# Kernel optimization log

Hardware: AMD Instinct MI355X
Metric: run time of the kernel (lower is better)

Reference implementation:

```python
import jax, jax.numpy as jnp
import numpy as np

N_NODES = 50000
N_EDGES = 800000
DIM = 100

def setup_inputs() -> dict:
    key = jax.random.key(0)
    k1, k2, k3, k4, k5, k6 = jax.random.split(key, 6)
    ego_embedding = jax.random.normal(k1, (N_NODES, DIM), dtype=jnp.float32)
    edge_src = jax.random.randint(k2, (N_EDGES,), 0, N_NODES, dtype=jnp.int32)
    edge_dst = jax.random.randint(k3, (N_EDGES,), 0, N_NODES, dtype=jnp.int32)
    edge_weight = jax.random.uniform(k4, (N_EDGES,), dtype=jnp.float32)
    W = jax.random.normal(k5, (DIM, DIM), dtype=jnp.float32) * (1.0 / np.sqrt(DIM))
    b = jax.random.normal(k6, (DIM,), dtype=jnp.float32) * 0.01
    return {"ego_embedding": ego_embedding, "edge_src": edge_src,
            "edge_dst": edge_dst, "edge_weight": edge_weight, "W": W, "b": b}

def reference(ego_embedding, edge_src, edge_dst, edge_weight, W, b):
    # Linear projection: h = x @ W^T + b  (torch Linear convention)
    hidden = ego_embedding @ W.T + b                    # [N, D]
    # u_mul_e: message on each edge = h[src] * edge_weight
    msgs = hidden[edge_src] * edge_weight[:, None]       # [E, D]
    # sum reduce into destination nodes
    out = jax.ops.segment_sum(msgs, edge_dst, num_segments=N_NODES)  # [N, D]
    return out
```

## Files before the change

kernel.cpp:

```cpp
#include <hip/hip_runtime.h>

#define N_NODES 50000
#define N_EDGES 800000
#define DIM 100

#define NB      1563
#define CAPB    768
#define OVF_CAP 4096
#define EPB     8192
#define GEMM_BLOCKS 625
#define BIN_BLOCKS  98
#define ROWS_PB 80

#define HIDB_OFF  0u
#define GCUR_OFF  10000000u
#define OVFC_OFF  10006256u
#define OVF_OFF   10006272u
#define BKT2_OFF  10071808u
#define WT_OFF    19674880u
#define WS_NEED   19714880u

__device__ inline unsigned bf16hi(float v) {
    unsigned u = __float_as_uint(v);
    u += 0x7FFFu + ((u >> 16) & 1u);
    return u & 0xFFFF0000u;
}
__device__ inline unsigned bf16pair(float lo, float hi) {
    unsigned ulo = __float_as_uint(lo); ulo += 0x7FFFu + ((ulo >> 16) & 1u);
    unsigned uhi = __float_as_uint(hi); uhi += 0x7FFFu + ((uhi >> 16) & 1u);
    return (ulo >> 16) | (uhi & 0xFFFF0000u);
}

__global__ __launch_bounds__(256) void srgnn_transpose(
    const float* __restrict__ W, float* __restrict__ Wt,
    int* __restrict__ gcur, int* __restrict__ ovfc)
{
    const unsigned i = blockIdx.x * 256u + threadIdx.x;
    if (i < DIM * DIM) {
        const int c = i / DIM, k = i - c * DIM;
        Wt[k * DIM + c] = W[i];
    }
    if (i < NB) gcur[i] = 0;
    if (i == 0) *ovfc = 0;
}

__global__ __launch_bounds__(512) void srgnn_gemm_bin(
    const float* __restrict__ x, const float* __restrict__ Wt,
    const float* __restrict__ b, unsigned* __restrict__ hidU,
    const int* __restrict__ esrc, const int* __restrict__ edst,
    const float* __restrict__ ew, int* __restrict__ gcur,
    int* __restrict__ ovfc, int4* __restrict__ ovf, uint2* __restrict__ bkt2)
{
    __shared__ __align__(16) char smem[32000];
    const int t = threadIdx.x;

    if (blockIdx.x < GEMM_BLOCKS) {
        float (*xs)[DIM] = (float (*)[DIM])smem;
        const int row0 = blockIdx.x * ROWS_PB;

        for (int i = t; i < ROWS_PB * 25; i += 512) {
            const int r = i / 25, c4 = (i - r * 25) * 4;
            const float4 v = *reinterpret_cast<const float4*>(
                &x[(size_t)(row0 + r) * DIM + c4]);
            *reinterpret_cast<float4*>(&xs[r][c4]) = v;
        }
        __syncthreads();

        if (t < 500) {
            const int g  = t / 25;
            const int c4 = (t - g * 25) * 4;
            const float4 bv = *reinterpret_cast<const float4*>(&b[c4]);
            float4 a0 = bv, a1 = bv, a2 = bv, a3 = bv;

            #pragma unroll 4
            for (int k = 0; k < DIM; ++k) {
                const float4 wv = *reinterpret_cast<const float4*>(&Wt[k * DIM + c4]);
                const float x0 = xs[g     ][k];
                const float x1 = xs[g + 20][k];
                const float x2 = xs[g + 40][k];
                const float x3 = xs[g + 60][k];
                a0.x += x0 * wv.x; a0.y += x0 * wv.y; a0.z += x0 * wv.z; a0.w += x0 * wv.w;
                a1.x += x1 * wv.x; a1.y += x1 * wv.y; a1.z += x1 * wv.z; a1.w += x1 * wv.w;
                a2.x += x2 * wv.x; a2.y += x2 * wv.y; a2.z += x2 * wv.z; a2.w += x2 * wv.w;
                a3.x += x3 * wv.x; a3.y += x3 * wv.y; a3.z += x3 * wv.z; a3.w += x3 * wv.w;
            }
            const int u0 = c4 >> 1;
            uint2 p;
            p.x = bf16pair(a0.x, a0.y); p.y = bf16pair(a0.z, a0.w);
            *reinterpret_cast<uint2*>(&hidU[(size_t)(row0 + g     ) * 50 + u0]) = p;
            p.x = bf16pair(a1.x, a1.y); p.y = bf16pair(a1.z, a1.w);
            *reinterpret_cast<uint2*>(&hidU[(size_t)(row0 + g + 20) * 50 + u0]) = p;
            p.x = bf16pair(a2.x, a2.y); p.y = bf16pair(a2.z, a2.w);
            *reinterpret_cast<uint2*>(&hidU[(size_t)(row0 + g + 40) * 50 + u0]) = p;
            p.x = bf16pair(a3.x, a3.y); p.y = bf16pair(a3.z, a3.w);
            *reinterpret_cast<uint2*>(&hidU[(size_t)(row0 + g + 60) * 50 + u0]) = p;
        }
    } else {
        int* hist = (int*)smem;
        int* lcur = hist + NB;
        const int e0 = (blockIdx.x - GEMM_BLOCKS) * EPB;

        for (int i = t; i < NB; i += 512) hist[i] = 0;
        __syncthreads();

        int d[16];
        #pragma unroll
        for (int k = 0; k < 16; ++k) {
            const int e = e0 + t + k * 512;
            d[k] = (e < N_EDGES) ? edst[e] : -1;
            if (d[k] >= 0) atomicAdd(&hist[d[k] >> 5], 1);
        }
        __syncthreads();
        for (int i = t; i < NB; i += 512)
            if (hist[i]) lcur[i] = atomicAdd(&gcur[i], hist[i]);
        __syncthreads();
        #pragma unroll
        for (int k = 0; k < 16; ++k) {
            if (d[k] >= 0) {
                const int e = e0 + t + k * 512;
                const int s = esrc[e];
                const float w = ew[e];
                const int bq = d[k] >> 5;
                const int pos = atomicAdd(&lcur[bq], 1);
                if (pos < CAPB) {
                    bkt2[(size_t)bq * CAPB + pos] =
                        make_uint2((unsigned)s | bf16hi(w), (unsigned)d[k]);
                } else {
                    const int op = atomicAdd(ovfc, 1);
                    if (op < OVF_CAP) ovf[op] = make_int4(d[k], s, __float_as_int(w), 0);
                }
            }
        }
    }
}

__global__ __launch_bounds__(256) void srgnn_agg_s32(
    const unsigned* __restrict__ hidU, const int* __restrict__ gcur,
    const uint2* __restrict__ bkt2, const int* __restrict__ ovfc,
    const int4* __restrict__ ovf, float* __restrict__ out)
{
    __shared__ uint2    recs[CAPB];
    __shared__ unsigned srt[CAPB];
    __shared__ int nh[32], sc[32], cur[32];

    const int t = threadIdx.x;
    const int bq = blockIdx.x;
    int cntb = gcur[bq];
    if (cntb > CAPB) cntb = CAPB;

    if (t < 32) nh[t] = 0;
    __syncthreads();
    for (int i = t; i < cntb; i += 256) {
        const uint2 r = bkt2[(size_t)bq * CAPB + i];
        recs[i] = r;
        atomicAdd(&nh[r.y & 31], 1);
    }
    __syncthreads();
    if (t < 32) sc[t] = nh[t];
    __syncthreads();
    for (int ofs = 1; ofs < 32; ofs <<= 1) {
        int a = 0;
        if (t < 32 && t >= ofs) a = sc[t - ofs];
        __syncthreads();
        if (t < 32) sc[t] += a;
        __syncthreads();
    }
    if (t < 32) cur[t] = sc[t] - nh[t];
    __syncthreads();
    for (int i = t; i < cntb; i += 256) {
        const uint2 r = recs[i];
        const int pos = atomicAdd(&cur[r.y & 31], 1);
        srt[pos] = r.x;
    }
    __syncthreads();

    int oc = *ovfc;
    if (oc > OVF_CAP) oc = OVF_CAP;
    const int lane = t & 63;
    const int wid  = t >> 6;
    const bool active = (lane < 50);

    for (int q = 0; q < 8; ++q) {
        const int n  = wid * 8 + q;
        const int s1 = sc[n];
        const int s0 = s1 - nh[n];
        float2 acc = make_float2(0.f, 0.f);

        int p = s0;
        for (; p + 8 <= s1; p += 8) {
            unsigned r[8], h[8];
            #pragma unroll
            for (int j = 0; j < 8; ++j) r[j] = srt[p + j];
            if (active) {
                #pragma unroll
                for (int j = 0; j < 8; ++j)
                    h[j] = hidU[(size_t)(r[j] & 0xFFFFu) * 50 + lane];
                #pragma unroll
                for (int j = 0; j < 8; ++j) {
                    const float wj = __uint_as_float(r[j] & 0xFFFF0000u);
                    acc.x += wj * __uint_as_float(h[j] << 16);
                    acc.y += wj * __uint_as_float(h[j] & 0xFFFF0000u);
                }
            }
        }
        for (; p < s1; ++p) {
            const unsigned r = srt[p];
            const float wi = __uint_as_float(r & 0xFFFF0000u);
            if (active) {
                const unsigned h = hidU[(size_t)(r & 0xFFFFu) * 50 + lane];
                acc.x += wi * __uint_as_float(h << 16);
                acc.y += wi * __uint_as_float(h & 0xFFFF0000u);
            }
        }

        const int ng = bq * 32 + n;
        if (oc > 0) {
            for (int i = 0; i < oc; ++i) {
                const int4 v = ovf[i];
                if (v.x == ng && active) {
                    const unsigned h = hidU[(size_t)v.y * 50 + lane];
                    const float wi = __int_as_float(v.z);
                    acc.x += wi * __uint_as_float(h << 16);
                    acc.y += wi * __uint_as_float(h & 0xFFFF0000u);
                }
            }
        }
        if (ng < N_NODES && active)
            *reinterpret_cast<float2*>(&out[(size_t)ng * DIM + 2 * lane]) = acc;
    }
}

__global__ __launch_bounds__(256) void srgnn_gemm_bias(
    const float* __restrict__ x, const float* __restrict__ W,
    const float* __restrict__ b, float* __restrict__ hidden)
{
    __shared__ float Wt[DIM][DIM + 4];
    __shared__ float bs[DIM];
    __shared__ float xs[8][DIM];
    const int t = threadIdx.x;
    for (int i = t; i < DIM * DIM; i += 256) {
        int c = i / DIM, k = i - c * DIM;
        Wt[k][c] = W[i];
    }
    if (t < DIM) bs[t] = b[t];
    const int row0 = blockIdx.x * 8;
    for (int i = t; i < 8 * DIM; i += 256) {
        int r = i / DIM, k = i - r * DIM;
        int row = row0 + r;
        xs[r][k] = (row < N_NODES) ? x[row * DIM + k] : 0.0f;
    }
    __syncthreads();
    if (t < 200) {
        const int r  = t / 25;
        const int c4 = (t - r * 25) * 4;
        float acc0 = bs[c4 + 0], acc1 = bs[c4 + 1], acc2 = bs[c4 + 2], acc3 = bs[c4 + 3];
        for (int k = 0; k < DIM; ++k) {
            const float xv = xs[r][k];
            const float4 wv = *reinterpret_cast<const float4*>(&Wt[k][c4]);
            acc0 += xv * wv.x; acc1 += xv * wv.y; acc2 += xv * wv.z; acc3 += xv * wv.w;
        }
        const int row = row0 + r;
        if (row < N_NODES)
            *reinterpret_cast<float4*>(&hidden[row * DIM + c4]) =
                make_float4(acc0, acc1, acc2, acc3);
    }
}

__global__ __launch_bounds__(256) void srgnn_scatter_atomic(
    const float* __restrict__ hidden, const int* __restrict__ esrc,
    const int* __restrict__ edst, const float* __restrict__ ew,
    float* __restrict__ out)
{
    const unsigned gid = blockIdx.x * 256u + threadIdx.x;
    const unsigned e = gid / 25u;
    const unsigned j = gid - e * 25u;
    if (e >= N_EDGES) return;
    const int   s  = esrc[e];
    const int   d  = edst[e];
    const float wt = ew[e];
    const float4 h = *reinterpret_cast<const float4*>(&hidden[(size_t)s * DIM + j * 4]);
    float* op = &out[(size_t)d * DIM + j * 4];
    atomicAdd(op + 0, h.x * wt);
    atomicAdd(op + 1, h.y * wt);
    atomicAdd(op + 2, h.z * wt);
    atomicAdd(op + 3, h.w * wt);
}

extern "C" void kernel_launch(void* const* d_in, const int* in_sizes, int n_in,
                              void* d_out, int out_size, void* d_ws, size_t ws_size,
                              hipStream_t stream) {
    const float* x    = (const float*)d_in[0];
    const int*   esrc = (const int*)  d_in[1];
    const int*   edst = (const int*)  d_in[2];
    const float* ew   = (const float*)d_in[3];
    const float* W    = (const float*)d_in[4];
    const float* b    = (const float*)d_in[5];
    float* out = (float*)d_out;

    char* ws = (char*)d_ws;

    if (ws_size >= WS_NEED) {
        unsigned* hidU = (unsigned*)(ws + HIDB_OFF);
        int*      gcur = (int*)     (ws + GCUR_OFF);
        int*      ovfc = (int*)     (ws + OVFC_OFF);
        int4*     ovf  = (int4*)    (ws + OVF_OFF);
        uint2*    bkt2 = (uint2*)   (ws + BKT2_OFF);
        float*    Wt   = (float*)   (ws + WT_OFF);

        srgnn_transpose<<<(DIM * DIM + 255) / 256, 256, 0, stream>>>(W, Wt, gcur, ovfc);
        srgnn_gemm_bin<<<GEMM_BLOCKS + BIN_BLOCKS, 512, 0, stream>>>(
            x, Wt, b, hidU, esrc, edst, ew, gcur, ovfc, ovf, bkt2);
        srgnn_agg_s32<<<NB, 256, 0, stream>>>(hidU, gcur, bkt2, ovfc, ovf, out);
    } else {
        float* hidden = (float*)ws;
        hipMemsetAsync(d_out, 0, (size_t)out_size * sizeof(float), stream);
        const int gemm_blocks = (N_NODES + 7) / 8;
        srgnn_gemm_bias<<<gemm_blocks, 256, 0, stream>>>(x, W, b, hidden);
        const long long work = (long long)N_EDGES * 25;
        const int scat_blocks = (int)((work + 255) / 256);
        srgnn_scatter_atomic<<<scat_blocks, 256, 0, stream>>>(hidden, esrc, edst, ew, out);
    }
}
```

Baseline: 72.90 us.

## Split edge binning into two-level radix passes and separate GEMM kernel

Replaces the single-pass binning into 1563 fine buckets with a two-level scheme: first bin edges into 98 coarse superbuckets (512 nodes each), then a second kernel splits each superbucket into 16 fine 32-node buckets. The aim is to cut global atomic contention and scattered writes across many buckets. The fused GEMM/bin kernel is also split into separate launches, with the GEMM using 40 rows per block and 256 threads. This adds an extra pass over the edge records and more kernel launches, and it no longer overlaps the GEMM with binning.

Measured after the change: 108.5 us. +48.9%, slower.

```diff
diff --git a/kernel.cpp b/kernel.cpp
--- a/kernel.cpp
+++ b/kernel.cpp
@@ -4,21 +4,25 @@
 #define N_EDGES 800000
 #define DIM 100
 
-#define NB      1563
-#define CAPB    768
-#define OVF_CAP 4096
-#define EPB     8192
-#define GEMM_BLOCKS 625
-#define BIN_BLOCKS  98
-#define ROWS_PB 80
+#define SB_COUNT 98
+#define CAP1     8704
+#define NB       1563
+#define NBP      1568
+#define CAPB     768
+#define OVF_CAP  4096
+#define EPB1     8192
+#define GEMM_BLOCKS 1250
+#define ROWS_PB  40
 
 #define HIDB_OFF  0u
-#define GCUR_OFF  10000000u
-#define OVFC_OFF  10006256u
-#define OVF_OFF   10006272u
-#define BKT2_OFF  10071808u
-#define WT_OFF    19674880u
-#define WS_NEED   19714880u
+#define G1_OFF    10000448u
+#define OVFC_OFF  10000448u+512u
+#define CNT2_OFF  10001024u
+#define OVF_OFF   10007296u
+#define BKT1_OFF  10072832u
+#define BKT2_OFF  16896768u
+#define WT_OFF    26530560u
+#define WS_NEED   26570560u
 
 __device__ inline unsigned bf16hi(float v) {
     unsigned u = __float_as_uint(v);
@@ -33,109 +37,157 @@
 
 __global__ __launch_bounds__(256) void srgnn_transpose(
     const float* __restrict__ W, float* __restrict__ Wt,
-    int* __restrict__ gcur, int* __restrict__ ovfc)
+    int* __restrict__ gcur1, int* __restrict__ ovfc)
 {
     const unsigned i = blockIdx.x * 256u + threadIdx.x;
     if (i < DIM * DIM) {
         const int c = i / DIM, k = i - c * DIM;
         Wt[k * DIM + c] = W[i];
     }
-    if (i < NB) gcur[i] = 0;
+    if (i < SB_COUNT) gcur1[i] = 0;
     if (i == 0) *ovfc = 0;
 }
 
-__global__ __launch_bounds__(512) void srgnn_gemm_bin(
+__global__ __launch_bounds__(256) void srgnn_gemm2b(
     const float* __restrict__ x, const float* __restrict__ Wt,
-    const float* __restrict__ b, unsigned* __restrict__ hidU,
+    const float* __restrict__ b, unsigned* __restrict__ hidU)
+{
+    __shared__ float xs[ROWS_PB][DIM];
+    const int t = threadIdx.x;
+    const int row0 = blockIdx.x * ROWS_PB;
+
+    for (int i = t; i < ROWS_PB * 25; i += 256) {
+        const int r = i / 25, c4 = (i - r * 25) * 4;
+        const float4 v = *reinterpret_cast<const float4*>(
+            &x[(size_t)(row0 + r) * DIM + c4]);
+        *reinterpret_cast<float4*>(&xs[r][c4]) = v;
+    }
+    __syncthreads();
+
+    if (t < 250) {
+        const int g  = t / 25;
+        const int c4 = (t - g * 25) * 4;
+        const float4 bv = *reinterpret_cast<const float4*>(&b[c4]);
+        float4 a0 = bv, a1 = bv, a2 = bv, a3 = bv;
+
+        #pragma unroll 4
+        for (int k = 0; k < DIM; ++k) {
+            const float4 wv = *reinterpret_cast<const float4*>(&Wt[k * DIM + c4]);
+            const float x0 = xs[g     ][k];
+            const float x1 = xs[g + 10][k];
+            const float x2 = xs[g + 20][k];
+            const float x3 = xs[g + 30][k];
+            a0.x += x0 * wv.x; a0.y += x0 * wv.y; a0.z += x0 * wv.z; a0.w += x0 * wv.w;
+            a1.x += x1 * wv.x; a1.y += x1 * wv.y; a1.z += x1 * wv.z; a1.w += x1 * wv.w;
+            a2.x += x2 * wv.x; a2.y += x2 * wv.y; a2.z += x2 * wv.z; a2.w += x2 * wv.w;
+            a3.x += x3 * wv.x; a3.y += x3 * wv.y; a3.z += x3 * wv.z; a3.w += x3 * wv.w;
+        }
+        const int u0 = c4 >> 1;
+        uint2 p;
+        p.x = bf16pair(a0.x, a0.y); p.y = bf16pair(a0.z, a0.w);
+        *reinterpret_cast<uint2*>(&hidU[(size_t)(row0 + g     ) * 50 + u0]) = p;
+        p.x = bf16pair(a1.x, a1.y); p.y = bf16pair(a1.z, a1.w);
+        *reinterpret_cast<uint2*>(&hidU[(size_t)(row0 + g + 10) * 50 + u0]) = p;
+        p.x = bf16pair(a2.x, a2.y); p.y = bf16pair(a2.z, a2.w);
+        *reinterpret_cast<uint2*>(&hidU[(size_t)(row0 + g + 20) * 50 + u0]) = p;
+        p.x = bf16pair(a3.x, a3.y); p.y = bf16pair(a3.z, a3.w);
+        *reinterpret_cast<uint2*>(&hidU[(size_t)(row0 + g + 30) * 50 + u0]) = p;
+    }
+}
+
+__global__ __launch_bounds__(512) void srgnn_bin1(
     const int* __restrict__ esrc, const int* __restrict__ edst,
-    const float* __restrict__ ew, int* __restrict__ gcur,
-    int* __restrict__ ovfc, int4* __restrict__ ovf, uint2* __restrict__ bkt2)
-{
-    __shared__ __align__(16) char smem[32000];
-    const int t = threadIdx.x;
-
-    if (blockIdx.x < GEMM_BLOCKS) {
-        float (*xs)[DIM] = (float (*)[DIM])smem;
-        const int row0 = blockIdx.x * ROWS_PB;
-
-        for (int i = t; i < ROWS_PB * 25; i += 512) {
-            const int r = i / 25, c4 = (i - r * 25) * 4;
-            const float4 v = *reinterpret_cast<const float4*>(
-                &x[(size_t)(row0 + r) * DIM + c4]);
-            *reinterpret_cast<float4*>(&xs[r][c4]) = v;
-        }
-        __syncthreads();
-
-        if (t < 500) {
-            const int g  = t / 25;
-            const int c4 = (t - g * 25) * 4;
-            const float4 bv = *reinterpret_cast<const float4*>(&b[c4]);
-            float4 a0 = bv, a1 = bv, a2 = bv, a3 = bv;
-
-            #pragma unroll 4
-            for (int k = 0; k < DIM; ++k) {
-                const float4 wv = *reinterpret_cast<const float4*>(&Wt[k * DIM + c4]);
-                const float x0 = xs[g     ][k];
-                const float x1 = xs[g + 20][k];
-                const float x2 = xs[g + 40][k];
-                const float x3 = xs[g + 60][k];
-                a0.x += x0 * wv.x; a0.y += x0 * wv.y; a0.z += x0 * wv.z; a0.w += x0 * wv.w;
-                a1.x += x1 * wv.x; a1.y += x1 * wv.y; a1.z += x1 * wv.z; a1.w += x1 * wv.w;
-                a2.x += x2 * wv.x; a2.y += x2 * wv.y; a2.z += x2 * wv.z; a2.w += x2 * wv.w;
-                a3.x += x3 * wv.x; a3.y += x3 * wv.y; a3.z += x3 * wv.z; a3.w += x3 * wv.w;
+    const float* __restrict__ ew, int* __restrict__ gcur1,
+    int* __restrict__ ovfc, int4* __restrict__ ovf, uint2* __restrict__ bkt1)
+{
+    __shared__ int hist[SB_COUNT];
+    __shared__ int lcur[SB_COUNT];
+    const int t = threadIdx.x;
+    const int e0 = blockIdx.x * EPB1;
+
+    for (int i = t; i < SB_COUNT; i += 512) hist[i] = 0;
+    __syncthreads();
+
+    int d[16];
+    #pragma unroll
+    for (int k = 0; k < 16; ++k) {
+        const int e = e0 + t + k * 512;
+        d[k] = (e < N_EDGES) ? edst[e] : -1;
+        if (d[k] >= 0) atomicAdd(&hist[d[k] >> 9], 1);
+    }
+    __syncthreads();
+    for (int i = t; i < SB_COUNT; i += 512)
+        if (hist[i]) lcur[i] = atomicAdd(&gcur1[i], hist[i]);
+    __syncthreads();
+    #pragma unroll
+    for (int k = 0; k < 16; ++k) {
+        if (d[k] >= 0) {
+            const int e = e0 + t + k * 512;
+            const int s = esrc[e];
+            const float w = ew[e];
+            const int sb = d[k] >> 9;
+            const int pos = atomicAdd(&lcur[sb], 1);
+            if (pos < CAP1) {
+                bkt1[(size_t)sb * CAP1 + pos] =
+                    make_uint2((unsigned)s | bf16hi(w), (unsigned)d[k]);
+            } else {
+                const int op = atomicAdd(ovfc, 1);
+                if (op < OVF_CAP) ovf[op] = make_int4(d[k], s, __float_as_int(w), 0);
             }
-            const int u0 = c4 >> 1;
-            uint2 p;
-            p.x = bf16pair(a0.x, a0.y); p.y = bf16pair(a0.z, a0.w);
-            *reinterpret_cast<uint2*>(&hidU[(size_t)(row0 + g     ) * 50 + u0]) = p;
-            p.x = bf16pair(a1.x, a1.y); p.y = bf16pair(a1.z, a1.w);
-            *reinterpret_cast<uint2*>(&hidU[(size_t)(row0 + g + 20) * 50 + u0]) = p;
-            p.x = bf16pair(a2.x, a2.y); p.y = bf16pair(a2.z, a2.w);
-            *reinterpret_cast<uint2*>(&hidU[(size_t)(row0 + g + 40) * 50 + u0]) = p;
-            p.x = bf16pair(a3.x, a3.y); p.y = bf16pair(a3.z, a3.w);
-            *reinterpret_cast<uint2*>(&hidU[(size_t)(row0 + g + 60) * 50 + u0]) = p;
-        }
-    } else {
-        int* hist = (int*)smem;
-        int* lcur = hist + NB;
-        const int e0 = (blockIdx.x - GEMM_BLOCKS) * EPB;
-
-        for (int i = t; i < NB; i += 512) hist[i] = 0;
-        __syncthreads();
-
-        int d[16];
+        }
+    }
+}
+
+__global__ __launch_bounds__(512) void srgnn_bin2(
+    const int* __restrict__ gcur1, const uint2* __restrict__ bkt1,
+    int* __restrict__ cnt2, int* __restrict__ ovfc, int4* __restrict__ ovf,
+    uint2* __restrict__ bkt2)
+{
+    __shared__ int histr[8][16];
+    const int t = threadIdx.x;
+    const int sb = blockIdx.x;
+    const int rep = t & 7;
+
+    int cnt = gcur1[sb];
+    if (cnt > CAP1) cnt = CAP1;
+
+    if (t < 128) histr[t >> 4][t & 15] = 0;
+    __syncthreads();
+
+    for (int i = t; i < cnt; i += 512) {
+        const uint2 r = bkt1[(size_t)sb * CAP1 + i];
+        atomicAdd(&histr[rep][(r.y >> 5) & 15], 1);
+    }
+    __syncthreads();
+
+    if (t < 16) {
+        int tot = 0;
+        int base[8];
         #pragma unroll
-        for (int k = 0; k < 16; ++k) {
-            const int e = e0 + t + k * 512;
-            d[k] = (e < N_EDGES) ? edst[e] : -1;
-            if (d[k] >= 0) atomicAdd(&hist[d[k] >> 5], 1);
-        }
-        __syncthreads();
-        for (int i = t; i < NB; i += 512)
-            if (hist[i]) lcur[i] = atomicAdd(&gcur[i], hist[i]);
-        __syncthreads();
+        for (int r = 0; r < 8; ++r) { base[r] = tot; tot += histr[r][t]; }
         #pragma unroll
-        for (int k = 0; k < 16; ++k) {
-            if (d[k] >= 0) {
-                const int e = e0 + t + k * 512;
-                const int s = esrc[e];
-                const float w = ew[e];
-                const int bq = d[k] >> 5;
-                const int pos = atomicAdd(&lcur[bq], 1);
-                if (pos < CAPB) {
-                    bkt2[(size_t)bq * CAPB + pos] =
-                        make_uint2((unsigned)s | bf16hi(w), (unsigned)d[k]);
-                } else {
-                    const int op = atomicAdd(ovfc, 1);
-                    if (op < OVF_CAP) ovf[op] = make_int4(d[k], s, __float_as_int(w), 0);
-                }
-            }
+        for (int r = 0; r < 8; ++r) histr[r][t] = base[r];
+        cnt2[sb * 16 + t] = (tot < CAPB) ? tot : CAPB;
+    }
+    __syncthreads();
+
+    for (int i = t; i < cnt; i += 512) {
+        const uint2 r = bkt1[(size_t)sb * CAP1 + i];
+        const int j = (r.y >> 5) & 15;
+        const int pos = atomicAdd(&histr[rep][j], 1);
+        if (pos < CAPB) {
+            bkt2[(size_t)(sb * 16 + j) * CAPB + pos] = r;
+        } else {
+            const int op = atomicAdd(ovfc, 1);
+            if (op < OVF_CAP)
+                ovf[op] = make_int4((int)r.y, (int)(r.x & 0xFFFFu),
+                                    (int)(r.x & 0xFFFF0000u), 0);
         }
     }
 }
 
 __global__ __launch_bounds__(256) void srgnn_agg_s32(
-    const unsigned* __restrict__ hidU, const int* __restrict__ gcur,
+    const unsigned* __restrict__ hidU, const int* __restrict__ cnt2,
     const uint2* __restrict__ bkt2, const int* __restrict__ ovfc,
     const int4* __restrict__ ovf, float* __restrict__ out)
 {
@@ -145,7 +197,7 @@
 
     const int t = threadIdx.x;
     const int bq = blockIdx.x;
-    int cntb = gcur[bq];
+    int cntb = cnt2[bq];
     if (cntb > CAPB) cntb = CAPB;
 
     if (t < 32) nh[t] = 0;
@@ -219,7 +271,7 @@
                 const int4 v = ovf[i];
                 if (v.x == ng && active) {
                     const unsigned h = hidU[(size_t)v.y * 50 + lane];
-                    const float wi = __int_as_float(v.z);
+                    const float wi = __uint_as_float((unsigned)v.z);
                     acc.x += wi * __uint_as_float(h << 16);
                     acc.y += wi * __uint_as_float(h & 0xFFFF0000u);
                 }
@@ -300,17 +352,21 @@
     char* ws = (char*)d_ws;
 
     if (ws_size >= WS_NEED) {
-        unsigned* hidU = (unsigned*)(ws + HIDB_OFF);
-        int*      gcur = (int*)     (ws + GCUR_OFF);
-        int*      ovfc = (int*)     (ws + OVFC_OFF);
-        int4*     ovf  = (int4*)    (ws + OVF_OFF);
-        uint2*    bkt2 = (uint2*)   (ws + BKT2_OFF);
-        float*    Wt   = (float*)   (ws + WT_OFF);
-
-        srgnn_transpose<<<(DIM * DIM + 255) / 256, 256, 0, stream>>>(W, Wt, gcur, ovfc);
-        srgnn_gemm_bin<<<GEMM_BLOCKS + BIN_BLOCKS, 512, 0, stream>>>(
-            x, Wt, b, hidU, esrc, edst, ew, gcur, ovfc, ovf, bkt2);
-        srgnn_agg_s32<<<NB, 256, 0, stream>>>(hidU, gcur, bkt2, ovfc, ovf, out);
+        unsigned* hidU  = (unsigned*)(ws + HIDB_OFF);
+        int*      gcur1 = (int*)     (ws + G1_OFF);
+        int*      ovfc  = (int*)     (ws + OVFC_OFF);
+        int*      cnt2  = (int*)     (ws + CNT2_OFF);
+        int4*     ovf   = (int4*)    (ws + OVF_OFF);
+        uint2*    bkt1  = (uint2*)   (ws + BKT1_OFF);
+        uint2*    bkt2  = (uint2*)   (ws + BKT2_OFF);
+        float*    Wt    = (float*)   (ws + WT_OFF);
+
+        srgnn_transpose<<<(DIM * DIM + 255) / 256, 256, 0, stream>>>(W, Wt, gcur1, ovfc);
+        srgnn_gemm2b<<<GEMM_BLOCKS, 256, 0, stream>>>(x, Wt, b, hidU);
+        srgnn_bin1<<<(N_EDGES + EPB1 - 1) / EPB1, 512, 0, stream>>>(
+            esrc, edst, ew, gcur1, ovfc, ovf, bkt1);
+        srgnn_bin2<<<SB_COUNT, 512, 0, stream>>>(gcur1, bkt1, cnt2, ovfc, ovf, bkt2);
+        srgnn_agg_s32<<<NB, 256, 0, stream>>>(hidU, cnt2, bkt2, ovfc, ovf, out);
     } else {
         float* hidden = (float*)ws;
         hipMemsetAsync(d_out, 0, (size_t)out_size * sizeof(float), stream);
```
